# Performance work log

Measured on AMD Instinct MI355X. Metric: run time of the kernel, lower is better.

Reference implementation:

```python
import jax, jax.numpy as jnp
import numpy as np

N_HD, N_DEL7, N_AVP, N_AVM = 100, 100, 50, 50
DT = 0.001
KAPPA_PHI, KAPPA_Y = 1.0, 1.0
AV_OFFSET = 0.0
ALPHA_TILDE = 10.0
# alpha used in the leak term inside forward():
ALPHA = ALPHA_TILDE + 0.5 * KAPPA_Y / KAPPA_PHI * 1.0 / (KAPPA_PHI + KAPPA_Y)  # 10.25
W_HD_HD_S = ALPHA_TILDE + 1.0 / (KAPPA_PHI + KAPPA_Y) - AV_OFFSET * KAPPA_Y / (KAPPA_Y + KAPPA_PHI)  # 10.5
W_HD_AV_S = np.sqrt(2.0) * KAPPA_Y / (KAPPA_Y + KAPPA_PHI)  # sqrt(2)/2
W_HD_D7_S = 1.0 / (KAPPA_PHI + KAPPA_Y)  # 0.5
W_AV_HD_S = 1.0
W_D7_HD_S = 1.0
TAU_AV = 0.01
TAU_D7 = 0.001


def _id_matr(x_to, x_from, sig):
    d = np.arccos(np.cos(x_to[:, None] - x_from[None, :]))
    M = np.exp(-0.5 * (d / sig) ** 2) / (np.sqrt(2.0 * np.pi) * sig)
    return M / M.sum(1)[0]


def _build_weights():
    p_hd = np.linspace(-np.pi, np.pi - 2 * np.pi / N_HD, N_HD)
    p_d7 = np.linspace(-np.pi, np.pi - 2 * np.pi / N_DEL7, N_DEL7)
    p_avp = np.linspace(-np.pi, np.pi - 2 * np.pi / N_AVP, N_AVP)
    p_avm = np.linspace(-np.pi, np.pi - 2 * np.pi / N_AVM, N_AVM)
    o, w0, w1 = -0.2, 0.0, 2.0
    W_HD_HD = 2.0 / N_HD * (o + np.maximum(0.0, w0 + w1 * np.cos(p_hd[:, None] - p_hd[None, :])))
    W_HD_AVplus = 2.0 / N_AVP * np.maximum(0.0, np.sin(p_hd[:, None] - p_avp[None, :] + np.pi / 4))
    W_HD_AVminus = 2.0 / N_AVM * np.maximum(0.0, -np.sin(p_hd[:, None] - p_avm[None, :] - np.pi / 4))
    W_AVplus_HD = _id_matr(p_avp, p_hd, 0.3)
    W_AVminus_HD = _id_matr(p_avm, p_hd, 0.3)
    d7w0, d7w1 = 0.5, -0.5
    W_Del7_HD = 2.0 / N_DEL7 * (d7w0 + d7w1 * np.cos(p_d7[:, None] - p_hd[None, :]))
    m0, m1 = 0.1, 0.0
    W_Del7_Del7 = 2.0 / N_DEL7 * (m0 + m1 * np.cos(p_d7[:, None] - p_d7[None, :]))
    j = np.pi / 2 * (1 - 2 * m0) / d7w0
    W_HD_Del7 = -j * _id_matr(p_hd, p_d7, 0.1)
    ws = dict(W_HD_HD=W_HD_HD, W_HD_AVplus=W_HD_AVplus, W_HD_AVminus=W_HD_AVminus,
              W_AVplus_HD=W_AVplus_HD, W_AVminus_HD=W_AVminus_HD,
              W_Del7_HD=W_Del7_HD, W_Del7_Del7=W_Del7_Del7, W_HD_Del7=W_HD_Del7)
    return {k: jnp.asarray(v, dtype=jnp.float32) for k, v in ws.items()}


def setup_inputs() -> dict:
    key = jax.random.key(0)
    k1, k2 = jax.random.split(key)
    B, S = 64, 5000
    inp = {
        'inputs': jax.random.normal(k1, (B, S, 2), dtype=jnp.float32),
        'r0': jax.random.uniform(k2, (1, B, N_HD + N_AVP + N_AVM + N_DEL7), dtype=jnp.float32),
    }
    inp.update(_build_weights())
    return inp


def reference(inputs, r0, W_HD_HD, W_HD_AVplus, W_HD_AVminus, W_AVplus_HD,
              W_AVminus_HD, W_Del7_HD, W_Del7_Del7, W_HD_Del7):
    # batch_first -> [seq, batch, 2]
    x = jnp.transpose(inputs, (1, 0, 2))
    r_HD0 = r0[0, :, :N_HD]
    r_AVp0 = r0[0, :, N_HD:N_HD + N_AVP]
    r_AVm0 = r0[0, :, N_HD + N_AVP:N_HD + N_AVP + N_AVM]
    r_D70 = r0[0, :, N_HD + N_AVP + N_AVM:]
    relu = jax.nn.relu

    def step(carry, x_t):
        r_HD, r_AVp, r_AVm, r_D7 = carry
        av = x_t[:, 1]  # [B]; HD input only feeds a dead input_term in the original
        r_HD_new = (r_HD
                    - ALPHA * r_HD * DT
                    + W_HD_HD_S * jnp.einsum('ij,bj->bi', W_HD_HD, r_HD) * DT
                    + W_HD_AV_S * jnp.einsum('ij,bj->bi', W_HD_AVplus, r_AVp) * DT
                    + W_HD_AV_S * jnp.einsum('ij,bj->bi', W_HD_AVminus, r_AVm) * DT
                    + W_HD_D7_S * jnp.einsum('ij,bj->bi', W_HD_Del7, relu(r_D7)) * r_HD * DT)
        gate_p = (av / DT + AV_OFFSET)[:, None]
        gate_m = (-av / DT + AV_OFFSET)[:, None]
        r_AVp_new = r_AVp + (1.0 / TAU_AV) * (-r_AVp + gate_p * W_AV_HD_S * jnp.einsum('ij,bj->bi', W_AVplus_HD, r_HD_new)) * DT
        r_AVm_new = r_AVm + (1.0 / TAU_AV) * (-r_AVm + gate_m * W_AV_HD_S * jnp.einsum('ij,bj->bi', W_AVminus_HD, r_HD_new)) * DT
        r_D7_new = r_D7 + (1.0 / TAU_D7) * (-r_D7
                                            + W_D7_HD_S * jnp.einsum('ij,bj->bi', W_Del7_HD, relu(r_HD_new))
                                            + jnp.einsum('ij,bj->bi', W_Del7_Del7, relu(r_D7))) * DT
        out = jnp.concatenate([r_HD_new, r_AVp_new, r_AVm_new, r_D7_new], axis=1)  # [B, 300]
        return (r_HD_new, r_AVp_new, r_AVm_new, r_D7_new), out

    carry, ys = jax.lax.scan(step, (r_HD0, r_AVp0, r_AVm0, r_D70), x)
    output = jnp.transpose(ys, (1, 0, 2))  # [B, S, 300] (batch_first)
    r_full_curr = jnp.concatenate(carry, axis=1)
    return output, r_full_curr
```

## Files before the change

### kernel.cpp

```cpp
#include <hip/hip_runtime.h>


#define SSTEPS 5000
#define PI_D 3.14159265358979323846

typedef float f2 __attribute__((ext_vector_type(2)));

__device__ __forceinline__ f2 pk_fma(f2 a, f2 b, f2 c) {
  f2 d;
  asm("v_pk_fma_f32 %0, %1, %2, %3" : "=v"(d) : "v"(a), "v"(b), "v"(c));
  return d;
}

template<int CTRL, int RM, bool BC>
__device__ __forceinline__ float dpp_mov_f(float x) {
  return __int_as_float(__builtin_amdgcn_update_dpp(0, __float_as_int(x), CTRL, RM, 0xF, BC));
}
__device__ __forceinline__ float scan16(float x) {
  x += dpp_mov_f<0x111,0xF,true>(x);
  x += dpp_mov_f<0x112,0xF,true>(x);
  x += dpp_mov_f<0x114,0xF,true>(x);
  x += dpp_mov_f<0x118,0xF,true>(x);
  return x;
}
__device__ __forceinline__ float scan8(float x) {
  x += dpp_mov_f<0x111,0xF,true>(x);
  x += dpp_mov_f<0x112,0xF,true>(x);
  x += dpp_mov_f<0x114,0xF,true>(x);
  return x;
}
__device__ __forceinline__ float wave_sum(float x) {
  x = scan16(x);
  x += dpp_mov_f<0x142,0xA,false>(x);
  x += dpp_mov_f<0x143,0xC,false>(x);
  return __int_as_float(__builtin_amdgcn_readlane(__float_as_int(x), 63));
}
__device__ __forceinline__ void bar_lgkm() {
  asm volatile("s_waitcnt lgkmcnt(0)\n\ts_barrier" ::: "memory");
}

__device__ __forceinline__ int neuron_of_pos(int pos) {
  if (pos < 100) return (pos >> 2) + 25 * (pos & 3);
  if (pos < 200) {
    int r = pos - 100, a = r >> 2, m = r & 3;
    return 100 + a + (m == 0 ? 0 : (m == 1 ? 50 : (m == 2 ? 25 : 75)));
  }
  return pos;
}
__device__ __forceinline__ int pos_of_neuron(int n) {
  if (n < 100) return 4 * (n % 25) + n / 25;
  if (n < 200) {
    int uu = n - 100, half = (uu >= 50) ? 1 : 0, w = uu - 50 * half;
    return 100 + 4 * (w % 25) + 2 * (w / 25) + half;
  }
  return n;
}

__global__
__attribute__((amdgpu_flat_work_group_size(512,512)))
__attribute__((amdgpu_waves_per_eu(2)))
void drosoph_rnn_kernel(
    const float* __restrict__ xin,
    const float* __restrict__ r0,
    const float* __restrict__ W_HD_HD,
    const float* __restrict__ W_HD_AVp,
    const float* __restrict__ W_HD_AVm,
    const float* __restrict__ W_AVp_HD,
    const float* __restrict__ W_AVm_HD,
    const float* __restrict__ W_D7_HD,
    const float* __restrict__ W_D7_D7,
    const float* __restrict__ W_HD_D7,
    float* __restrict__ out)
{
  const int b    = blockIdx.x;
  const int t    = threadIdx.x;
  const int lane = t & 63;
  const int wid  = t >> 6;

  __shared__ __align__(16) float su[2][328];
  __shared__ float avb[SSTEPS];
  __shared__ float d7r[104];

  const bool p1  = (t < 400);
  const int  g   = t >> 4;
  const int  r1  = t & 15;
  const bool pav = (t < 200);
  const int  ai  = t >> 3;
  const int  qa  = t & 7;
  const bool w7  = (wid == 7);

  const float kAV = 0.70710678118654752f;

  f2 w1p[4][10];
  if (p1) {
    #pragma unroll
    for (int k = 0; k < 4; ++k) {
      const int o = g + 25*k;
      #pragma unroll
      for (int q = 0; q < 20; ++q) {
        const int pos = 20*r1 + q;
        const int n   = neuron_of_pos(pos);
        float w = 0.0f;
        if      (n < 100) w = 10.5f * W_HD_HD [o*100 + n];
        else if (n < 150) w = kAV   * W_HD_AVp[o*50 + (n-100)];
        else if (n < 200) w = kAV   * W_HD_AVm[o*50 + (n-150)];
        else if (n < 300) w = 0.5f  * W_HD_D7 [o*100 + (n-200)];
        w1p[k][q >> 1][q & 1] = w;
      }
    }
  }

  f2 wavK[2][8];
  if (pav) {
    #pragma unroll
    for (int m = 0; m < 2; ++m) {
      const int a2 = ai + 25*m;
      #pragma unroll
      for (int u = 0; u < 4; ++u) {
        #pragma unroll
        for (int mm = 0; mm < 4; ++mm) {
          const int pos = 4*(qa + 8*u) + mm;
          float w = 0.0f;
          if (pos < 100) w = W_AVp_HD[a2*100 + neuron_of_pos(pos)];
          wavK[m][2*u + (mm >> 1)][mm & 1] = w;
        }
      }
    }
  }

  float cw0=0.f, cw1=0.f, sw0=0.f, sw1=0.f, m0w=0.f, m1w=0.f;
  float cdA=0.f, sdA=0.f, cdB=0.f, sdB=0.f;
  if (w7) {
    if (lane < 50) {
      const int n0 = neuron_of_pos(2*lane);
      const int n1 = neuron_of_pos(2*lane + 1);
      m0w = 1.0f; m1w = 1.0f;
      double pj0 = -PI_D + n0*(2.0*PI_D/100.0);
      double pj1 = -PI_D + n1*(2.0*PI_D/100.0);
      cw0 = (float)cos(pj0);  sw0 = (float)sin(pj0);
      cw1 = (float)cos(pj1);  sw1 = (float)sin(pj1);
    }
    double pA = -PI_D + lane     *(2.0*PI_D/100.0);
    double pB = -PI_D + (lane+64)*(2.0*PI_D/100.0);
    cdA = (float)cos(pA); sdA = (float)sin(pA);
    cdB = (float)cos(pB); sdB = (float)sin(pB);
  }

  if (t < 328) { su[0][t] = 0.f; su[1][t] = 0.f; }
  if (t < 104) d7r[t] = 0.f;
  {
    const float2* x2 = (const float2*)xin + (size_t)b * SSTEPS;
    for (int i = t; i < SSTEPS; i += 512) avb[i] = x2[i].y;
  }
  if (t < 300) {
    float v = r0[b*300 + t];
    if (t >= 200) v = fmaxf(v, 0.f);
    su[0][pos_of_neuron(t)] = v;
  }
  __syncthreads();

  float* outb = out + (size_t)b * ((size_t)SSTEPS * 300);
  int p = 0;

  #pragma unroll 1
  for (int s = 0; s < SSTEPS; ++s) {
    const float* suc = su[p];
    float*       sun = su[p^1];
    float T0loc = 0.f;

    if (p1) {
      f2 vv2[10];
      {
        const float4* vp = (const float4*)(suc + 20*r1);
        float4 V0=vp[0], V1=vp[1], V2=vp[2], V3=vp[3], V4=vp[4];
        vv2[0] = f2{V0.x, V0.y}; vv2[1] = f2{V0.z, V0.w};
        vv2[2] = f2{V1.x, V1.y}; vv2[3] = f2{V1.z, V1.w};
        vv2[4] = f2{V2.x, V2.y}; vv2[5] = f2{V2.z, V2.w};
        vv2[6] = f2{V3.x, V3.y}; vv2[7] = f2{V3.z, V3.w};
        vv2[8] = f2{V4.x, V4.y}; vv2[9] = f2{V4.z, V4.w};
      }
      const float4 hd4 = *(const float4*)(suc + 4*g);
      f2 c0={0.f,0.f}, c1={0.f,0.f}, c2={0.f,0.f}, c3={0.f,0.f};
      #pragma unroll
      for (int q2 = 0; q2 < 10; ++q2) {
        c0 = pk_fma(w1p[0][q2], vv2[q2], c0);
        c1 = pk_fma(w1p[1][q2], vv2[q2], c1);
        c2 = pk_fma(w1p[2][q2], vv2[q2], c2);
        c3 = pk_fma(w1p[3][q2], vv2[q2], c3);
      }
      float e0 = c0[0]+c0[1], e1 = c1[0]+c1[1];
      float e2 = c2[0]+c2[1], e3 = c3[0]+c3[1];
      if (r1 >= 10) { e0 *= hd4.x; e1 *= hd4.y; e2 *= hd4.z; e3 *= hd4.w; }
      e0 = scan16(e0); e1 = scan16(e1); e2 = scan16(e2); e3 = scan16(e3);
      if (r1 == 15) {
        float h0 = fmaf(0.001f, fmaf(-10.25f, hd4.x, e0), hd4.x);
        float h1 = fmaf(0.001f, fmaf(-10.25f, hd4.y, e1), hd4.y);
        float h2 = fmaf(0.001f, fmaf(-10.25f, hd4.z, e2), hd4.z);
        float h3 = fmaf(0.001f, fmaf(-10.25f, hd4.w, e3), hd4.w);
        *(float4*)(sun + 4*g) = make_float4(h0, h1, h2, h3);
      }
    } else if (w7) {
      float x = 0.f;
      if (lane < 50) { float2 z = *(const float2*)(suc + 200 + 2*lane); x = z.x + z.y; }
      T0loc = wave_sum(x);
      if (s > 0) {
        float* od = outb + (size_t)(s-1) * 300;
        #pragma unroll
        for (int u = 0; u < 5; ++u) {
          const int idx = lane + 64*u;
          if (idx < 300) {
            float v;
            if (idx < 100) {
              v = suc[4*(idx % 25) + idx/25];
            } else if (idx < 200) {
              const int uu = idx - 100, half = (uu >= 50) ? 1 : 0;
              const int w_ = uu - 50*half;
              v = suc[100 + 4*(w_ % 25) + 2*(w_/25) + half];
            } else {
              v = d7r[idx - 200];
            }
            od[idx] = v;
          }
        }
      }
    }
    bar_lgkm();

    if (pav) {
      const float4* hp = (const float4*)sun;
      float4 H0 = hp[qa], H1 = hp[qa+8], H2 = hp[qa+16], H3 = hp[qa+24];
      f2 hh2[8];
      hh2[0] = f2{H0.x, H0.y}; hh2[1] = f2{H0.z, H0.w};
      hh2[2] = f2{H1.x, H1.y}; hh2[3] = f2{H1.z, H1.w};
      hh2[4] = f2{H2.x, H2.y}; hh2[5] = f2{H2.z, H2.w};
      hh2[6] = f2{H3.x, H3.y}; hh2[7] = f2{H3.z, H3.w};
      f2 d0 = f2{0.f,0.f}, d1 = f2{0.f,0.f};
      #pragma unroll
      for (int u = 0; u < 8; ++u) {
        d0 = pk_fma(wavK[0][u], hh2[u], d0);
        d1 = pk_fma(wavK[1][u], hh2[u], d1);
      }
      const float s0v = scan8(d0[0] + d0[1]);
      const float s1v = scan8(d1[0] + d1[1]);
      if (qa == 7) {
        const float gp  = avb[s] * 1000.0f;
        const float4 av4 = *(const float4*)(suc + 100 + 4*ai);
        const float np0 = fmaf(0.1f, fmaf(gp,  s0v, -av4.x), av4.x);
        const float nm0 = fmaf(0.1f, fmaf(-gp, s0v, -av4.y), av4.y);
        const float np1 = fmaf(0.1f, fmaf(gp,  s1v, -av4.z), av4.z);
        const float nm1 = fmaf(0.1f, fmaf(-gp, s1v, -av4.w), av4.w);
        *(float4*)(sun + 100 + 4*ai) = make_float4(np0, nm0, np1, nm1);
      }
    } else if (w7) {
      float2 y2 = *(const float2*)(sun + 2*lane);
      float y0 = fmaxf(y2.x, 0.f), y1 = fmaxf(y2.y, 0.f);
      float pS0 = fmaf(m1w, y1, m0w * y0);
      float pC  = fmaf(cw1, y1, cw0 * y0);
      float pS  = fmaf(sw1, y1, sw0 * y0);
      float S0 = wave_sum(pS0);
      float C  = wave_sum(pC);
      float S  = wave_sum(pS);
      float base = fmaf(0.002f, T0loc, 0.01f * S0);
      {
        float d7 = base - 0.01f * fmaf(cdA, C, sdA * S);
        sun[200+lane] = fmaxf(d7, 0.f);
        d7r[lane]     = d7;
      }
      if (lane < 36) {
        float d7 = base - 0.01f * fmaf(cdB, C, sdB * S);
        sun[264+lane] = fmaxf(d7, 0.f);
        d7r[64+lane]  = d7;
      }
    }
    bar_lgkm();
    p ^= 1;
  }

  if (t < 300) {
    float v;
    if (t < 100) {
      v = su[p][4*(t % 25) + t/25];
    } else if (t < 200) {
      const int uu = t - 100, half = (uu >= 50) ? 1 : 0;
      const int w_ = uu - 50*half;
      v = su[p][100 + 4*(w_ % 25) + 2*(w_/25) + half];
    } else {
      v = d7r[t - 200];
    }
    outb[(size_t)(SSTEPS-1) * 300 + t] = v;
    out[(size_t)64 * SSTEPS * 300 + (size_t)b * 300 + t] = v;
  }
}

extern "C" void kernel_launch(void* const* d_in, const int* in_sizes, int n_in,
                              void* d_out, int out_size, void* d_ws, size_t ws_size,
                              hipStream_t stream) {
  drosoph_rnn_kernel<<<64, 512, 0, stream>>>(
      (const float*)d_in[0],
      (const float*)d_in[1],
      (const float*)d_in[2],
      (const float*)d_in[3],
      (const float*)d_in[4],
      (const float*)d_in[5],
      (const float*)d_in[6],
      (const float*)d_in[7],
      (const float*)d_in[8],
      (const float*)d_in[9],
      (float*)d_out);
}
```

Measured before the change: 3.911 ms.

## Pack two batch elements per workgroup with 200 threads each for matvecs

```diff
diff --git a/kernel.cpp b/kernel.cpp
--- a/kernel.cpp
+++ b/kernel.cpp
@@ -29,11 +29,11 @@
   x += dpp_mov_f<0x114,0xF,true>(x);
   return x;
 }
-__device__ __forceinline__ float wave_sum(float x) {
+__device__ __forceinline__ float wave_sum48(float x) {
   x = scan16(x);
-  x += dpp_mov_f<0x142,0xA,false>(x);
-  x += dpp_mov_f<0x143,0xC,false>(x);
-  return __int_as_float(__builtin_amdgcn_readlane(__float_as_int(x), 63));
+  x += dpp_mov_f<0x142,0x2,false>(x);
+  x += dpp_mov_f<0x143,0x4,false>(x);
+  return __int_as_float(__builtin_amdgcn_readlane(__float_as_int(x), 47));
 }
 __device__ __forceinline__ void bar_lgkm() {
   asm volatile("s_waitcnt lgkmcnt(0)\n\ts_barrier" ::: "memory");
@@ -72,33 +72,31 @@
     const float* __restrict__ W_HD_D7,
     float* __restrict__ out)
 {
-  const int b    = blockIdx.x;
+  const int bid  = blockIdx.x;
   const int t    = threadIdx.x;
-  const int lane = t & 63;
-  const int wid  = t >> 6;
-
-  __shared__ __align__(16) float su[2][328];
-  __shared__ float avb[SSTEPS];
-  __shared__ float d7r[104];
-
-  const bool p1  = (t < 400);
-  const int  g   = t >> 4;
-  const int  r1  = t & 15;
-  const bool pav = (t < 200);
-  const int  ai  = t >> 3;
-  const int  qa  = t & 7;
-  const bool w7  = (wid == 7);
+  const int bb   = t >> 8;
+  const int L    = t & 255;
+  const int b    = 2*bid + bb;
+
+  __shared__ __align__(16) float su[2][2][328];
+  __shared__ float avb[2][SSTEPS];
+  __shared__ float d7r[2][104];
+
+  const bool aux = (L < 56);
+  const bool mv  = (L >= 56);
+  const int  mg  = (L - 56) >> 3;
+  const int  mq  = (L - 56) & 7;
 
   const float kAV = 0.70710678118654752f;
 
-  f2 w1p[4][10];
-  if (p1) {
+  f2 w1p[4][20];
+  if (mv) {
     #pragma unroll
     for (int k = 0; k < 4; ++k) {
-      const int o = g + 25*k;
+      const int o = mg + 25*k;
       #pragma unroll
-      for (int q = 0; q < 20; ++q) {
-        const int pos = 20*r1 + q;
+      for (int q = 0; q < 40; ++q) {
+        const int pos = 40*mq + q;
         const int n   = neuron_of_pos(pos);
         float w = 0.0f;
         if      (n < 100) w = 10.5f * W_HD_HD [o*100 + n];
@@ -111,15 +109,15 @@
   }
 
   f2 wavK[2][8];
-  if (pav) {
+  if (mv) {
     #pragma unroll
     for (int m = 0; m < 2; ++m) {
-      const int a2 = ai + 25*m;
+      const int a2 = mg + 25*m;
       #pragma unroll
       for (int u = 0; u < 4; ++u) {
         #pragma unroll
         for (int mm = 0; mm < 4; ++mm) {
-          const int pos = 4*(qa + 8*u) + mm;
+          const int pos = 4*(mq + 8*u) + mm;
           float w = 0.0f;
           if (pos < 100) w = W_AVp_HD[a2*100 + neuron_of_pos(pos)];
           wavK[m][2*u + (mm >> 1)][mm & 1] = w;
@@ -128,96 +126,110 @@
     }
   }
 
-  float cw0=0.f, cw1=0.f, sw0=0.f, sw1=0.f, m0w=0.f, m1w=0.f;
-  float cdA=0.f, sdA=0.f, cdB=0.f, sdB=0.f;
-  if (w7) {
-    if (lane < 50) {
-      const int n0 = neuron_of_pos(2*lane);
-      const int n1 = neuron_of_pos(2*lane + 1);
-      m0w = 1.0f; m1w = 1.0f;
-      double pj0 = -PI_D + n0*(2.0*PI_D/100.0);
-      double pj1 = -PI_D + n1*(2.0*PI_D/100.0);
-      cw0 = (float)cos(pj0);  sw0 = (float)sin(pj0);
-      cw1 = (float)cos(pj1);  sw1 = (float)sin(pj1);
-    }
-    double pA = -PI_D + lane     *(2.0*PI_D/100.0);
-    double pB = -PI_D + (lane+64)*(2.0*PI_D/100.0);
-    cdA = (float)cos(pA); sdA = (float)sin(pA);
-    cdB = (float)cos(pB); sdB = (float)sin(pB);
-  }
-
-  if (t < 328) { su[0][t] = 0.f; su[1][t] = 0.f; }
-  if (t < 104) d7r[t] = 0.f;
-  {
-    const float2* x2 = (const float2*)xin + (size_t)b * SSTEPS;
-    for (int i = t; i < SSTEPS; i += 512) avb[i] = x2[i].y;
-  }
-  if (t < 300) {
-    float v = r0[b*300 + t];
-    if (t >= 200) v = fmaxf(v, 0.f);
-    su[0][pos_of_neuron(t)] = v;
+  int posA = 0, posB = 0, posC = 0;
+  float cw0=0,cw1=0,cw2=0,sw0=0,sw1=0,sw2=0;
+  float cdA=0,sdA=0,cdB=0,sdB=0;
+  if (aux) {
+    if (L < 48) {
+      posA = pos_of_neuron(L);
+      posB = pos_of_neuron(L+48);
+      posC = (L < 4) ? pos_of_neuron(L+96) : posA;
+      double p0 = -PI_D + L     *(2.0*PI_D/100.0);
+      double p1 = -PI_D + (L+48)*(2.0*PI_D/100.0);
+      cw0=(float)cos(p0); sw0=(float)sin(p0);
+      cw1=(float)cos(p1); sw1=(float)sin(p1);
+      if (L < 4) {
+        double p2 = -PI_D + (L+96)*(2.0*PI_D/100.0);
+        cw2=(float)cos(p2); sw2=(float)sin(p2);
+      }
+    }
+    if (L < 50) {
+      double pa = -PI_D + (2*L)  *(2.0*PI_D/100.0);
+      double pb = -PI_D + (2*L+1)*(2.0*PI_D/100.0);
+      cdA=(float)cos(pa); sdA=(float)sin(pa);
+      cdB=(float)cos(pb); sdB=(float)sin(pb);
+    }
+  }
+
+  for (int i = t; i < 2*2*328;  i += 512) (&su[0][0][0])[i] = 0.f;
+  for (int i = t; i < 2*104;    i += 512) (&d7r[0][0])[i]   = 0.f;
+  for (int i = t; i < 2*SSTEPS; i += 512) {
+    int b2 = i / SSTEPS, s2 = i - b2*SSTEPS;
+    const float2* x2 = (const float2*)xin + (size_t)(2*bid + b2)*SSTEPS;
+    avb[b2][s2] = x2[s2].y;
+  }
+  for (int i = t; i < 600; i += 512) {
+    int b2 = i / 300, n = i - b2*300;
+    float v = r0[(size_t)(2*bid + b2)*300 + n];
+    if (n >= 200) v = fmaxf(v, 0.f);
+    su[b2][0][pos_of_neuron(n)] = v;
   }
   __syncthreads();
 
-  float* outb = out + (size_t)b * ((size_t)SSTEPS * 300);
+  float*       outb = out + (size_t)b * ((size_t)SSTEPS*300);
+  const float* avbb = avb[bb];
+  float*       d7rb = d7r[bb];
   int p = 0;
 
   #pragma unroll 1
   for (int s = 0; s < SSTEPS; ++s) {
-    const float* suc = su[p];
-    float*       sun = su[p^1];
+    const float* sucb = su[bb][p];
+    float*       sunb = su[bb][p^1];
     float T0loc = 0.f;
 
-    if (p1) {
-      f2 vv2[10];
-      {
-        const float4* vp = (const float4*)(suc + 20*r1);
-        float4 V0=vp[0], V1=vp[1], V2=vp[2], V3=vp[3], V4=vp[4];
-        vv2[0] = f2{V0.x, V0.y}; vv2[1] = f2{V0.z, V0.w};
-        vv2[2] = f2{V1.x, V1.y}; vv2[3] = f2{V1.z, V1.w};
-        vv2[4] = f2{V2.x, V2.y}; vv2[5] = f2{V2.z, V2.w};
-        vv2[6] = f2{V3.x, V3.y}; vv2[7] = f2{V3.z, V3.w};
-        vv2[8] = f2{V4.x, V4.y}; vv2[9] = f2{V4.z, V4.w};
-      }
-      const float4 hd4 = *(const float4*)(suc + 4*g);
-      f2 c0={0.f,0.f}, c1={0.f,0.f}, c2={0.f,0.f}, c3={0.f,0.f};
+    if (mv) {
+      const float4* vp  = (const float4*)(sucb + 40*mq);
+      const float4  hd4 = *(const float4*)(sucb + 4*mg);
+      f2 cX0={0,0},cX1={0,0},cX2={0,0},cX3={0,0};
+      f2 cY0={0,0},cY1={0,0},cY2={0,0},cY3={0,0};
       #pragma unroll
-      for (int q2 = 0; q2 < 10; ++q2) {
-        c0 = pk_fma(w1p[0][q2], vv2[q2], c0);
-        c1 = pk_fma(w1p[1][q2], vv2[q2], c1);
-        c2 = pk_fma(w1p[2][q2], vv2[q2], c2);
-        c3 = pk_fma(w1p[3][q2], vv2[q2], c3);
-      }
-      float e0 = c0[0]+c0[1], e1 = c1[0]+c1[1];
-      float e2 = c2[0]+c2[1], e3 = c3[0]+c3[1];
-      if (r1 >= 10) { e0 *= hd4.x; e1 *= hd4.y; e2 *= hd4.z; e3 *= hd4.w; }
-      e0 = scan16(e0); e1 = scan16(e1); e2 = scan16(e2); e3 = scan16(e3);
-      if (r1 == 15) {
+      for (int r = 0; r < 10; ++r) {
+        float4 V = vp[r];
+        f2 vlo = f2{V.x, V.y}, vhi = f2{V.z, V.w};
+        cX0 = pk_fma(w1p[0][2*r],   vlo, cX0);
+        cY0 = pk_fma(w1p[0][2*r+1], vhi, cY0);
+        cX1 = pk_fma(w1p[1][2*r],   vlo, cX1);
+        cY1 = pk_fma(w1p[1][2*r+1], vhi, cY1);
+        cX2 = pk_fma(w1p[2][2*r],   vlo, cX2);
+        cY2 = pk_fma(w1p[2][2*r+1], vhi, cY2);
+        cX3 = pk_fma(w1p[3][2*r],   vlo, cX3);
+        cY3 = pk_fma(w1p[3][2*r+1], vhi, cY3);
+      }
+      float e0 = (cX0[0]+cX0[1]) + (cY0[0]+cY0[1]);
+      float e1 = (cX1[0]+cX1[1]) + (cY1[0]+cY1[1]);
+      float e2 = (cX2[0]+cX2[1]) + (cY2[0]+cY2[1]);
+      float e3 = (cX3[0]+cX3[1]) + (cY3[0]+cY3[1]);
+      if (mq >= 5) { e0 *= hd4.x; e1 *= hd4.y; e2 *= hd4.z; e3 *= hd4.w; }
+      e0 = scan8(e0); e1 = scan8(e1); e2 = scan8(e2); e3 = scan8(e3);
+      if (mq == 7) {
         float h0 = fmaf(0.001f, fmaf(-10.25f, hd4.x, e0), hd4.x);
         float h1 = fmaf(0.001f, fmaf(-10.25f, hd4.y, e1), hd4.y);
         float h2 = fmaf(0.001f, fmaf(-10.25f, hd4.z, e2), hd4.z);
         float h3 = fmaf(0.001f, fmaf(-10.25f, hd4.w, e3), hd4.w);
-        *(float4*)(sun + 4*g) = make_float4(h0, h1, h2, h3);
-      }
-    } else if (w7) {
+        *(float4*)(sunb + 4*mg) = make_float4(h0, h1, h2, h3);
+      }
+    } else {
       float x = 0.f;
-      if (lane < 50) { float2 z = *(const float2*)(suc + 200 + 2*lane); x = z.x + z.y; }
-      T0loc = wave_sum(x);
+      if (L < 48) {
+        x = sucb[200+L] + sucb[248+L];
+        if (L < 4) x += sucb[296+L];
+      }
+      T0loc = wave_sum48(x);
       if (s > 0) {
-        float* od = outb + (size_t)(s-1) * 300;
+        float* od = outb + (size_t)(s-1)*300;
         #pragma unroll
-        for (int u = 0; u < 5; ++u) {
-          const int idx = lane + 64*u;
+        for (int u = 0; u < 6; ++u) {
+          int idx = L + 56*u;
           if (idx < 300) {
             float v;
             if (idx < 100) {
-              v = suc[4*(idx % 25) + idx/25];
+              v = sucb[4*(idx % 25) + idx/25];
             } else if (idx < 200) {
               const int uu = idx - 100, half = (uu >= 50) ? 1 : 0;
               const int w_ = uu - 50*half;
-              v = suc[100 + 4*(w_ % 25) + 2*(w_/25) + half];
+              v = sucb[100 + 4*(w_ % 25) + 2*(w_/25) + half];
             } else {
-              v = d7r[idx - 200];
+              v = d7rb[idx - 200];
             }
             od[idx] = v;
           }
@@ -226,9 +238,9 @@
     }
     bar_lgkm();
 
-    if (pav) {
-      const float4* hp = (const float4*)sun;
-      float4 H0 = hp[qa], H1 = hp[qa+8], H2 = hp[qa+16], H3 = hp[qa+24];
+    if (mv) {
+      const float4* hp = (const float4*)sunb;
+      float4 H0 = hp[mq], H1 = hp[mq+8], H2 = hp[mq+16], H3 = hp[mq+24];
       f2 hh2[8];
       hh2[0] = f2{H0.x, H0.y}; hh2[1] = f2{H0.z, H0.w};
       hh2[2] = f2{H1.x, H1.y}; hh2[3] = f2{H1.z, H1.w};
@@ -242,60 +254,64 @@
       }
       const float s0v = scan8(d0[0] + d0[1]);
       const float s1v = scan8(d1[0] + d1[1]);
-      if (qa == 7) {
-        const float gp  = avb[s] * 1000.0f;
-        const float4 av4 = *(const float4*)(suc + 100 + 4*ai);
+      if (mq == 7) {
+        const float gp  = avbb[s] * 1000.0f;
+        const float4 av4 = *(const float4*)(sucb + 100 + 4*mg);
         const float np0 = fmaf(0.1f, fmaf(gp,  s0v, -av4.x), av4.x);
         const float nm0 = fmaf(0.1f, fmaf(-gp, s0v, -av4.y), av4.y);
         const float np1 = fmaf(0.1f, fmaf(gp,  s1v, -av4.z), av4.z);
         const float nm1 = fmaf(0.1f, fmaf(-gp, s1v, -av4.w), av4.w);
-        *(float4*)(sun + 100 + 4*ai) = make_float4(np0, nm0, np1, nm1);
-      }
-    } else if (w7) {
-      float2 y2 = *(const float2*)(sun + 2*lane);
-      float y0 = fmaxf(y2.x, 0.f), y1 = fmaxf(y2.y, 0.f);
-      float pS0 = fmaf(m1w, y1, m0w * y0);
-      float pC  = fmaf(cw1, y1, cw0 * y0);
-      float pS  = fmaf(sw1, y1, sw0 * y0);
-      float S0 = wave_sum(pS0);
-      float C  = wave_sum(pC);
-      float S  = wave_sum(pS);
+        *(float4*)(sunb + 100 + 4*mg) = make_float4(np0, nm0, np1, nm1);
+      }
+    } else {
+      float y0 = 0.f, y1 = 0.f, y2 = 0.f;
+      if (L < 48) {
+        y0 = fmaxf(sunb[posA], 0.f);
+        y1 = fmaxf(sunb[posB], 0.f);
+        y2 = (L < 4) ? fmaxf(sunb[posC], 0.f) : 0.f;
+      }
+      float pS0 = (y0 + y1) + y2;
+      float pC  = cw0*y0 + cw1*y1 + cw2*y2;
+      float pS  = sw0*y0 + sw1*y1 + sw2*y2;
+      float S0 = wave_sum48(pS0);
+      float C  = wave_sum48(pC);
+      float S  = wave_sum48(pS);
       float base = fmaf(0.002f, T0loc, 0.01f * S0);
-      {
-        float d7 = base - 0.01f * fmaf(cdA, C, sdA * S);
-        sun[200+lane] = fmaxf(d7, 0.f);
-        d7r[lane]     = d7;
-      }
-      if (lane < 36) {
-        float d7 = base - 0.01f * fmaf(cdB, C, sdB * S);
-        sun[264+lane] = fmaxf(d7, 0.f);
-        d7r[64+lane]  = d7;
+      if (L < 50) {
+        float da = base - 0.01f * fmaf(cdA, C, sdA * S);
+        float db = base - 0.01f * fmaf(cdB, C, sdB * S);
+        *(float2*)(sunb + 200 + 2*L) = make_float2(fmaxf(da, 0.f), fmaxf(db, 0.f));
+        *(float2*)(d7rb + 2*L)       = make_float2(da, db);
       }
     }
     bar_lgkm();
     p ^= 1;
   }
 
-  if (t < 300) {
-    float v;
-    if (t < 100) {
-      v = su[p][4*(t % 25) + t/25];
-    } else if (t < 200) {
-      const int uu = t - 100, half = (uu >= 50) ? 1 : 0;
-      const int w_ = uu - 50*half;
-      v = su[p][100 + 4*(w_ % 25) + 2*(w_/25) + half];
-    } else {
-      v = d7r[t - 200];
-    }
-    outb[(size_t)(SSTEPS-1) * 300 + t] = v;
-    out[(size_t)64 * SSTEPS * 300 + (size_t)b * 300 + t] = v;
+  #pragma unroll
+  for (int u = 0; u < 2; ++u) {
+    int idx = L + 256*u;
+    if (idx < 300) {
+      float v;
+      if (idx < 100) {
+        v = su[bb][p][4*(idx % 25) + idx/25];
+      } else if (idx < 200) {
+        const int uu = idx - 100, half = (uu >= 50) ? 1 : 0;
+        const int w_ = uu - 50*half;
+        v = su[bb][p][100 + 4*(w_ % 25) + 2*(w_/25) + half];
+      } else {
+        v = d7rb[idx - 200];
+      }
+      outb[(size_t)(SSTEPS-1)*300 + idx] = v;
+      out[(size_t)64*SSTEPS*300 + (size_t)b*300 + idx] = v;
+    }
   }
 }
 
 extern "C" void kernel_launch(void* const* d_in, const int* in_sizes, int n_in,
                               void* d_out, int out_size, void* d_ws, size_t ws_size,
                               hipStream_t stream) {
-  drosoph_rnn_kernel<<<64, 512, 0, stream>>>(
+  drosoph_rnn_kernel<<<32, 512, 0, stream>>>(
       (const float*)d_in[0],
       (const float*)d_in[1],
       (const float*)d_in[2],
```

After: 7.639 ms. +95.3%, slower.
